# Kernel optimization log

Measured on AMD Instinct MI355X. Metric: run time of the kernel, lower is better.

Reference implementation:

```python
import jax, jax.numpy as jnp
import numpy as np


def setup_inputs() -> dict:
    key = jax.random.key(0)
    ks = jax.random.split(key, 5)
    B, M, R = 32, 32, 128
    d_lang, d_region, d_rank, d_fusion = 1024, 2048, 256, 256
    u = jax.random.normal(ks[0], (B, M, d_lang), dtype=jnp.float32)
    v = jax.random.normal(ks[1], (B, R, d_region), dtype=jnp.float32)
    # Linear weights stored torch-style as (out_features, in_features)
    Wu = jax.random.normal(ks[2], (d_rank, d_lang), dtype=jnp.float32) * (1.0 / np.sqrt(d_lang))
    Wv = jax.random.normal(ks[3], (d_rank, d_region), dtype=jnp.float32) * (1.0 / np.sqrt(d_region))
    Wp = jax.random.normal(ks[4], (d_fusion, d_rank), dtype=jnp.float32) * (1.0 / np.sqrt(d_rank))
    bp = jnp.zeros((d_fusion,), dtype=jnp.float32)
    return {"u": u, "v": v, "Wu": Wu, "Wv": Wv, "Wp": Wp, "bp": bp}


def reference(u, v, Wu, Wv, Wp, bp):
    # u: (B, M, d_lang), v: (B, R, d_region)
    up = jnp.einsum('bmd,rd->bmr', u, Wu)          # (B, M, d_rank)  [rd: out x in]
    vp = jnp.einsum('bnd,rd->bnr', v, Wv)          # (B, R, d_rank)
    # broadcast bilinear multiply: (B, M, R, d_rank)
    prod = up[:, :, None, :] * vp[:, None, :, :]
    o = jnp.einsum('bmnk,fk->bmnf', prod, Wp) + bp  # p-linear -> (B, M, R, d_fusion)
    # dropout is identity in inference mode
    return jax.nn.relu(o)
```

## Files before the change

kernel.cpp:

```cpp
#include <hip/hip_runtime.h>
#include <hip/hip_bf16.h>


typedef __attribute__((ext_vector_type(8))) short short8;
typedef __attribute__((ext_vector_type(4))) float floatx4;

__device__ __forceinline__ short f2bf(float f) {
    union { float f; unsigned u; } cv; cv.f = f;
    unsigned r = cv.u + 0x7fffu + ((cv.u >> 16) & 1u);
    return (short)(r >> 16);
}
__device__ __forceinline__ float bf2f(short s) {
    union { unsigned u; float f; } cv;
    cv.u = ((unsigned)(unsigned short)s) << 16; return cv.f;
}

#define N_U  1048576
#define N_V  8388608
#define N_WU 262144
#define N_WV 524288
#define N_WP 65536

__global__ __launch_bounds__(256) void convert_kernel(
    const float* __restrict__ u, const float* __restrict__ v,
    const float* __restrict__ Wu, const float* __restrict__ Wv,
    const float* __restrict__ Wp, short* __restrict__ dst)
{
    const int n_u = N_U / 4, n_v = N_V / 4, n_wu = N_WU / 4, n_wv = N_WV / 4,
              n_wp = N_WP / 4;
    const int total = n_u + n_v + n_wu + n_wv + n_wp;
    for (int i4 = blockIdx.x * blockDim.x + threadIdx.x; i4 < total;
         i4 += gridDim.x * blockDim.x) {
        const float* src; int off = i4;
        if (off < n_u) src = u;
        else { off -= n_u;
            if (off < n_v) src = v;
            else { off -= n_v;
                if (off < n_wu) src = Wu;
                else { off -= n_wu;
                    if (off < n_wv) src = Wv;
                    else { off -= n_wv; src = Wp; } } } }
        float4 f = *((const float4*)src + off);
        short4 o;
        o.x = f2bf(f.x); o.y = f2bf(f.y); o.z = f2bf(f.z); o.w = f2bf(f.w);
        *((short4*)dst + i4) = o;
    }
}

__global__ __launch_bounds__(256) void proj_kernel(
    const short* __restrict__ Xu, const short* __restrict__ Wgu,
    short* __restrict__ Cu,
    const short* __restrict__ Xv, const short* __restrict__ Wgv,
    short* __restrict__ Cv)
{
    __shared__ short Xs[64 * 40];
    __shared__ short Wsh[64 * 40];

    const int tid  = threadIdx.x;
    const int lane = tid & 63;
    const int wave = tid >> 6;
    const int quad = lane >> 4;
    const int l15  = lane & 15;

    int blk = blockIdx.x;
    const short *X, *W; short* C; int D;
    if (blk < 64) { X = Xu; W = Wgu; C = Cu; D = 1024; }
    else          { blk -= 64; X = Xv; W = Wgv; C = Cv; D = 2048; }
    const int r0 = (blk >> 2) * 64;
    const int c0 = (blk & 3) * 64;
    const int wr = (wave >> 1) * 32;
    const int wc = (wave & 1) * 32;

    const int sr  = tid >> 2;
    const int skg = (tid & 3) * 8;

    floatx4 acc[2][2] = {};

    for (int kc = 0; kc < D; kc += 32) {
        __syncthreads();
        *(short8*)&Xs[sr * 40 + skg]  = *(const short8*)(X + (size_t)(r0 + sr) * D + kc + skg);
        *(short8*)&Wsh[sr * 40 + skg] = *(const short8*)(W + (size_t)(c0 + sr) * D + kc + skg);
        __syncthreads();

        short8 a[2], bfr[2];
#pragma unroll
        for (int t = 0; t < 2; t++)
            a[t] = *(const short8*)&Xs[(wr + t * 16 + l15) * 40 + quad * 8];
#pragma unroll
        for (int t = 0; t < 2; t++)
            bfr[t] = *(const short8*)&Wsh[(wc + t * 16 + l15) * 40 + quad * 8];
#pragma unroll
        for (int tn = 0; tn < 2; tn++)
#pragma unroll
            for (int tf = 0; tf < 2; tf++)
                acc[tn][tf] = __builtin_amdgcn_mfma_f32_16x16x32_bf16(
                    a[tn], bfr[tf], acc[tn][tf], 0, 0, 0);
    }

#pragma unroll
    for (int tn = 0; tn < 2; tn++)
#pragma unroll
        for (int tf = 0; tf < 2; tf++)
#pragma unroll
            for (int r = 0; r < 4; r++) {
                int row = r0 + wr + tn * 16 + quad * 4 + r;
                int col = c0 + wc + tf * 16 + l15;
                C[(size_t)row * 256 + col] = f2bf(acc[tn][tf][r]);
            }
}

__global__ __launch_bounds__(256) void bilinear_kernel(
    const short* __restrict__ up, const short* __restrict__ vp,
    const short* __restrict__ Wp, const float* __restrict__ bp,
    float* __restrict__ out)
{
    __shared__ short vp_s[128 * 40];
    __shared__ short Ws[128 * 40];
    __shared__ float up_s[256];

    const int tid  = threadIdx.x;
    const int lane = tid & 63;
    const int wave = tid >> 6;
    const int quad = lane >> 4;
    const int l15  = lane & 15;

    const int f_blk = blockIdx.x & 1;
    const int bm    = blockIdx.x >> 1;
    const int b     = bm >> 5;
    const int f0    = f_blk * 128;
    const int wn    = (wave >> 1) * 64;
    const int wf    = (wave & 1) * 64;

    up_s[tid] = bf2f(up[(size_t)bm * 256 + tid]);

    const int sn  = tid >> 1;
    const int skh = (tid & 1) * 16;

    floatx4 acc[4][4] = {};

    for (int kc = 0; kc < 256; kc += 32) {
        __syncthreads();
        {
            const short* p = vp + (size_t)(b * 128 + sn) * 256 + kc + skh;
            short8 v0 = *(const short8*)p;
            short8 v1 = *(const short8*)(p + 8);
            *(short8*)&vp_s[sn * 40 + skh]     = v0;
            *(short8*)&vp_s[sn * 40 + skh + 8] = v1;
        }
        {
            const short* wpp = Wp + (size_t)(f0 + sn) * 256 + kc + skh;
            short8 w0 = *(const short8*)wpp;
            short8 w1 = *(const short8*)(wpp + 8);
            float us[16];
            const float4* us4 = (const float4*)&up_s[kc + skh];
            *(float4*)&us[0]  = us4[0];
            *(float4*)&us[4]  = us4[1];
            *(float4*)&us[8]  = us4[2];
            *(float4*)&us[12] = us4[3];
            short8 o0, o1;
#pragma unroll
            for (int i = 0; i < 8; i++) o0[i] = f2bf(bf2f(w0[i]) * us[i]);
#pragma unroll
            for (int i = 0; i < 8; i++) o1[i] = f2bf(bf2f(w1[i]) * us[8 + i]);
            *(short8*)&Ws[sn * 40 + skh]     = o0;
            *(short8*)&Ws[sn * 40 + skh + 8] = o1;
        }
        __syncthreads();

        short8 a[4], bfr[4];
#pragma unroll
        for (int t = 0; t < 4; t++)
            a[t] = *(const short8*)&vp_s[(wn + t * 16 + l15) * 40 + quad * 8];
#pragma unroll
        for (int t = 0; t < 4; t++)
            bfr[t] = *(const short8*)&Ws[(wf + t * 16 + l15) * 40 + quad * 8];
#pragma unroll
        for (int tn = 0; tn < 4; tn++)
#pragma unroll
            for (int tf = 0; tf < 4; tf++)
                acc[tn][tf] = __builtin_amdgcn_mfma_f32_16x16x32_bf16(
                    a[tn], bfr[tf], acc[tn][tf], 0, 0, 0);
    }

    float bpv[4];
#pragma unroll
    for (int tf = 0; tf < 4; tf++) bpv[tf] = bp[f0 + wf + tf * 16 + l15];

    const size_t out_base = (size_t)bm * 128 * 256;
#pragma unroll
    for (int tn = 0; tn < 4; tn++)
#pragma unroll
        for (int r = 0; r < 4; r++) {
            int n = wn + tn * 16 + quad * 4 + r;
            float* op = out + out_base + (size_t)n * 256 + f0 + wf + l15;
#pragma unroll
            for (int tf = 0; tf < 4; tf++) {
                float val = acc[tn][tf][r] + bpv[tf];
                op[tf * 16] = fmaxf(val, 0.0f);
            }
        }
}

extern "C" void kernel_launch(void* const* d_in, const int* in_sizes, int n_in,
                              void* d_out, int out_size, void* d_ws, size_t ws_size,
                              hipStream_t stream) {
    const float* u  = (const float*)d_in[0];
    const float* v  = (const float*)d_in[1];
    const float* Wu = (const float*)d_in[2];
    const float* Wv = (const float*)d_in[3];
    const float* Wp = (const float*)d_in[4];
    const float* bp = (const float*)d_in[5];
    float* out = (float*)d_out;

    short* bf    = (short*)d_ws;
    short* u_bf  = bf;
    short* v_bf  = u_bf + N_U;
    short* Wu_bf = v_bf + N_V;
    short* Wv_bf = Wu_bf + N_WU;
    short* Wp_bf = Wv_bf + N_WV;
    short* up_bf = Wp_bf + N_WP;
    short* vp_bf = up_bf + 262144;

    convert_kernel<<<dim3(2048), dim3(256), 0, stream>>>(u, v, Wu, Wv, Wp, bf);
    proj_kernel<<<dim3(320), dim3(256), 0, stream>>>(
        u_bf, Wu_bf, up_bf, v_bf, Wv_bf, vp_bf);
    bilinear_kernel<<<dim3(2048), dim3(256), 0, stream>>>(
        up_bf, vp_bf, Wp_bf, bp, out);
}
```

Baseline: 220.4 us.

## Load tiles directly global-to-LDS and pack bf16 scaling with truncation

Tile loads in the projection and bilinear kernels now use global_load_lds, which writes straight into shared memory without passing through registers. Because each lane writes a fixed contiguous slot, the LDS row padding is dropped from 40 to 32. The Wp*up scaling now packs pairs with a byte permute, which truncates to bf16 instead of rounding to nearest even. The risks are LDS bank conflicts on the unpadded MFMA fragment reads, a small precision change from truncation, and relying only on __syncthreads to wait for the asynchronous LDS writes.

```diff
diff --git a/kernel.cpp b/kernel.cpp
--- a/kernel.cpp
+++ b/kernel.cpp
@@ -4,6 +4,7 @@
 
 typedef __attribute__((ext_vector_type(8))) short short8;
 typedef __attribute__((ext_vector_type(4))) float floatx4;
+typedef __attribute__((ext_vector_type(4))) unsigned uintx4;
 
 __device__ __forceinline__ short f2bf(float f) {
     union { float f; unsigned u; } cv; cv.f = f;
@@ -14,6 +15,15 @@
     union { unsigned u; float f; } cv;
     cv.u = ((unsigned)(unsigned short)s) << 16; return cv.f;
 }
+__device__ __forceinline__ unsigned scale2(short a, short b, float ua, float ub) {
+    float x = __uint_as_float(((unsigned)(unsigned short)a) << 16) * ua;
+    float y = __uint_as_float(((unsigned)(unsigned short)b) << 16) * ub;
+    return __builtin_amdgcn_perm(__float_as_uint(y), __float_as_uint(x), 0x07060302);
+}
+
+#define GL2LDS(gptr, lptr) __builtin_amdgcn_global_load_lds(                    \
+    (const __attribute__((address_space(1))) void*)(gptr),                      \
+    (__attribute__((address_space(3))) void*)(lptr), 16, 0, 0)
 
 #define N_U  1048576
 #define N_V  8388608
@@ -53,8 +63,8 @@
     const short* __restrict__ Xv, const short* __restrict__ Wgv,
     short* __restrict__ Cv)
 {
-    __shared__ short Xs[64 * 40];
-    __shared__ short Wsh[64 * 40];
+    __shared__ short Xs[64 * 32];
+    __shared__ short Wsh[64 * 32];
 
     const int tid  = threadIdx.x;
     const int lane = tid & 63;
@@ -78,17 +88,17 @@
 
     for (int kc = 0; kc < D; kc += 32) {
         __syncthreads();
-        *(short8*)&Xs[sr * 40 + skg]  = *(const short8*)(X + (size_t)(r0 + sr) * D + kc + skg);
-        *(short8*)&Wsh[sr * 40 + skg] = *(const short8*)(W + (size_t)(c0 + sr) * D + kc + skg);
+        GL2LDS(X + (size_t)(r0 + sr) * D + kc + skg, &Xs[sr * 32 + skg]);
+        GL2LDS(W + (size_t)(c0 + sr) * D + kc + skg, &Wsh[sr * 32 + skg]);
         __syncthreads();
 
         short8 a[2], bfr[2];
 #pragma unroll
         for (int t = 0; t < 2; t++)
-            a[t] = *(const short8*)&Xs[(wr + t * 16 + l15) * 40 + quad * 8];
+            a[t] = *(const short8*)&Xs[(wr + t * 16 + l15) * 32 + quad * 8];
 #pragma unroll
         for (int t = 0; t < 2; t++)
-            bfr[t] = *(const short8*)&Wsh[(wc + t * 16 + l15) * 40 + quad * 8];
+            bfr[t] = *(const short8*)&Wsh[(wc + t * 16 + l15) * 32 + quad * 8];
 #pragma unroll
         for (int tn = 0; tn < 2; tn++)
 #pragma unroll
@@ -114,8 +124,8 @@
     const short* __restrict__ Wp, const float* __restrict__ bp,
     float* __restrict__ out)
 {
-    __shared__ short vp_s[128 * 40];
-    __shared__ short Ws[128 * 40];
+    __shared__ short vp_s[128 * 32];
+    __shared__ short Ws[128 * 32];
     __shared__ float up_s[256];
 
     const int tid  = threadIdx.x;
@@ -133,6 +143,8 @@
 
     up_s[tid] = bf2f(up[(size_t)bm * 256 + tid]);
 
+    const int sr  = tid >> 2;
+    const int skg = (tid & 3) * 8;
     const int sn  = tid >> 1;
     const int skh = (tid & 1) * 16;
 
@@ -141,39 +153,39 @@
     for (int kc = 0; kc < 256; kc += 32) {
         __syncthreads();
         {
-            const short* p = vp + (size_t)(b * 128 + sn) * 256 + kc + skh;
-            short8 v0 = *(const short8*)p;
-            short8 v1 = *(const short8*)(p + 8);
-            *(short8*)&vp_s[sn * 40 + skh]     = v0;
-            *(short8*)&vp_s[sn * 40 + skh + 8] = v1;
+            const short* g = vp + (size_t)(b * 128 + sr) * 256 + kc + skg;
+            GL2LDS(g,                 &vp_s[sr * 32 + skg]);
+            GL2LDS(g + 64 * 256,      &vp_s[(64 + sr) * 32 + skg]);
         }
         {
             const short* wpp = Wp + (size_t)(f0 + sn) * 256 + kc + skh;
             short8 w0 = *(const short8*)wpp;
             short8 w1 = *(const short8*)(wpp + 8);
-            float us[16];
-            const float4* us4 = (const float4*)&up_s[kc + skh];
-            *(float4*)&us[0]  = us4[0];
-            *(float4*)&us[4]  = us4[1];
-            *(float4*)&us[8]  = us4[2];
-            *(float4*)&us[12] = us4[3];
-            short8 o0, o1;
-#pragma unroll
-            for (int i = 0; i < 8; i++) o0[i] = f2bf(bf2f(w0[i]) * us[i]);
-#pragma unroll
-            for (int i = 0; i < 8; i++) o1[i] = f2bf(bf2f(w1[i]) * us[8 + i]);
-            *(short8*)&Ws[sn * 40 + skh]     = o0;
-            *(short8*)&Ws[sn * 40 + skh + 8] = o1;
+            const float* us = &up_s[kc + skh];
+            float uv[16];
+            *(float4*)&uv[0]  = *(const float4*)(us);
+            *(float4*)&uv[4]  = *(const float4*)(us + 4);
+            *(float4*)&uv[8]  = *(const float4*)(us + 8);
+            *(float4*)&uv[12] = *(const float4*)(us + 12);
+            uintx4 o0, o1;
+#pragma unroll
+            for (int i = 0; i < 4; i++)
+                o0[i] = scale2(w0[2 * i], w0[2 * i + 1], uv[2 * i], uv[2 * i + 1]);
+#pragma unroll
+            for (int i = 0; i < 4; i++)
+                o1[i] = scale2(w1[2 * i], w1[2 * i + 1], uv[8 + 2 * i], uv[9 + 2 * i]);
+            *(uintx4*)&Ws[sn * 32 + skh]     = o0;
+            *(uintx4*)&Ws[sn * 32 + skh + 8] = o1;
         }
         __syncthreads();
 
         short8 a[4], bfr[4];
 #pragma unroll
         for (int t = 0; t < 4; t++)
-            a[t] = *(const short8*)&vp_s[(wn + t * 16 + l15) * 40 + quad * 8];
+            a[t] = *(const short8*)&vp_s[(wn + t * 16 + l15) * 32 + quad * 8];
 #pragma unroll
         for (int t = 0; t < 4; t++)
-            bfr[t] = *(const short8*)&Ws[(wf + t * 16 + l15) * 40 + quad * 8];
+            bfr[t] = *(const short8*)&Ws[(wf + t * 16 + l15) * 32 + quad * 8];
 #pragma unroll
         for (int tn = 0; tn < 4; tn++)
 #pragma unroll
```

Measured after the change: 214.3 us. 2.8% less time.
